# Kernel optimization log

Hardware: AMD Instinct MI355X
Metric: run time of the kernel (lower is better)

Reference implementation:

```python
import jax, jax.numpy as jnp
import numpy as np


def setup_inputs() -> dict:
    key = jax.random.key(0)
    ks = jax.random.split(key, 9)
    b, t_q, t_k, n_q, n_k = 4, 128, 512, 512, 512
    out_size = 512
    s = 0.02  # small init scale for weights
    return {
        "query": jax.random.normal(ks[0], (b, t_q, n_q), jnp.float32),
        "keys": jax.random.normal(ks[1], (b, t_k, n_k), jnp.float32),
        "values": jax.random.normal(ks[2], (b, t_k, n_k), jnp.float32),
        "W_q": jax.random.normal(ks[3], (n_k, n_q), jnp.float32) * s,
        "b_q": jnp.zeros((n_k,), jnp.float32),
        "w_att": jax.random.normal(ks[4], (n_k,), jnp.float32) * s,
        "b_att": jnp.zeros((1,), jnp.float32),
        "W_out": jax.random.normal(ks[5], (out_size, n_q + n_k), jnp.float32) * s,
        "b_out": jnp.zeros((out_size,), jnp.float32),
    }


def reference(query, keys, values, W_q, b_q, w_att, b_att, W_out, b_out):
    # linear_q: [b, t_q, query_size] -> [b, t_q, key_size]
    att_query = jnp.einsum("bqd,nd->bqn", query, W_q) + b_q
    # Bahdanau additive score: tanh(q + k) projected by linear_att (key_size -> 1)
    # intermediate: [b, t_q, t_k, n]
    sum_qk = jnp.tanh(att_query[:, :, None, :] + keys[:, None, :, :])
    scores = jnp.einsum("bqkn,n->bqk", sum_qk, w_att) + b_att[0]
    # mask is None by default; dropout p=0 -> identity
    probs = jax.nn.softmax(scores, axis=-1)  # [b, t_q, t_k]
    context = jnp.einsum("bqk,bkn->bqn", probs, values)
    # linear_out on concat([query, context]) + tanh nonlinearity
    cat = jnp.concatenate([query, context], axis=-1)
    out = jnp.tanh(jnp.einsum("bqc,oc->bqo", cat, W_out) + b_out)
    return out, probs
```

## Files before the change

### kernel.cpp

```cpp
#include <hip/hip_runtime.h>
#include <hip/hip_fp16.h>


#define BB    4
#define TQ    128
#define TK    512
#define NN    512
#define OUTSZ 512
#define CATSZ 1024
#define K2E   2.8853900817779268f
#define L2E   1.4426950408889634f
#define MAT   262144
#define WS_HALVES (11 * MAT)

typedef __attribute__((ext_vector_type(4))) _Float16 half4;
typedef __attribute__((ext_vector_type(8))) _Float16 half8;
typedef __attribute__((ext_vector_type(2))) _Float16 h2;

#if __has_builtin(__builtin_amdgcn_exp2f)
#define EXP2F(x) __builtin_amdgcn_exp2f(x)
#else
#define EXP2F(x) exp2f(x)
#endif
#if __has_builtin(__builtin_amdgcn_rcpf)
#define RCPF(x) __builtin_amdgcn_rcpf(x)
#else
#define RCPF(x) (1.0f / (x))
#endif

__device__ __forceinline__ h2 u2h(unsigned int u) {
  union { unsigned int i; h2 h; } v; v.i = u; return v.h;
}
__device__ __forceinline__ half4 uu2h4(unsigned int a, unsigned int b) {
  union { uint2 u; half4 h; } c; c.u = make_uint2(a, b); return c.h;
}
#if __has_builtin(__builtin_amdgcn_fdot2)
__device__ __forceinline__ float FDOT2(h2 a, h2 b, float c) {
  return __builtin_amdgcn_fdot2(a, b, c, false);
}
#else
__device__ __forceinline__ float FDOT2(h2 a, h2 b, float c) {
  return fmaf((float)a.x, (float)b.x, fmaf((float)a.y, (float)b.y, c));
}
#endif

__device__ __forceinline__ float fast_tanh(float x) {
  float e = EXP2F(x * K2E);
  return fmaf(-2.0f, RCPF(e + 1.0f), 1.0f);
}
__device__ __forceinline__ float waveRedSum(float s) {
  #pragma unroll
  for (int m = 32; m >= 1; m >>= 1) s += __shfl_xor(s, m, 64);
  return s;
}
__device__ __forceinline__ float fma4(float4 w, float4 v, float acc) {
  acc = fmaf(w.x, v.x, acc); acc = fmaf(w.y, v.y, acc);
  acc = fmaf(w.z, v.z, acc); acc = fmaf(w.w, v.w, acc);
  return acc;
}
__device__ __forceinline__ float4 scqh(float4 s, half4 E, float A, float w) {
  s.x = fmaf(w, RCPF(fmaf((float)E.x, A, 1.0f)), s.x);
  s.y = fmaf(w, RCPF(fmaf((float)E.y, A, 1.0f)), s.y);
  s.z = fmaf(w, RCPF(fmaf((float)E.z, A, 1.0f)), s.z);
  s.w = fmaf(w, RCPF(fmaf((float)E.w, A, 1.0f)), s.w);
  return s;
}
__device__ __forceinline__ void dotq(float4& r0, float4& r1, uint4 wp, unsigned int cpa, unsigned int cpb) {
  h2 c0 = u2h(cpa), c1 = u2h(cpb);
  r0.x = FDOT2(u2h(wp.x), c0, r0.x); r1.x = FDOT2(u2h(wp.x), c1, r1.x);
  r0.y = FDOT2(u2h(wp.y), c0, r0.y); r1.y = FDOT2(u2h(wp.y), c1, r1.y);
  r0.z = FDOT2(u2h(wp.z), c0, r0.z); r1.z = FDOT2(u2h(wp.z), c1, r1.z);
  r0.w = FDOT2(u2h(wp.w), c0, r0.w); r1.w = FDOT2(u2h(wp.w), c1, r1.w);
}

__global__ __launch_bounds__(256)
void pack_kernel(const float* __restrict__ keys, const float* __restrict__ W_q,
                 const float* __restrict__ W_out, const float* __restrict__ values,
                 _Float16* __restrict__ ws)
{
  __shared__ float tile[32][33];
  const int idx = blockIdx.x;
  const int tx = threadIdx.x & 31, ty = threadIdx.x >> 5;

  if (idx >= 1792) {
    int r = idx - 1792;
    int b = r >> 8, k2 = r & 255;
    const float* r0 = values + ((size_t)b * 512 + 2 * k2) * 512;
    const float* r1 = r0 + 512;
    int n0 = threadIdx.x * 2;
    float2 a = *(const float2*)(r0 + n0);
    float2 c = *(const float2*)(r1 + n0);
    _Float16* dst = ws + (size_t)7 * MAT + (size_t)b * MAT + k2 * 1024 + n0 * 2;
    half4 h = {(_Float16)a.x, (_Float16)c.x, (_Float16)a.y, (_Float16)c.y};
    *(half4*)dst = h;
    return;
  }

  if (idx < 1024) {
    int b = idx >> 8, r = idx & 255;
    int by = r >> 4, bx = r & 15;
    const float* src = keys + (size_t)b * MAT;
    _Float16* dst = ws + (size_t)b * MAT;
    #pragma unroll
    for (int i = 0; i < 32; i += 8)
      tile[ty + i][tx] = src[(size_t)(by * 32 + ty + i) * 512 + bx * 32 + tx] * K2E;
    __syncthreads();
    #pragma unroll
    for (int i = 0; i < 32; i += 8)
      dst[(size_t)(bx * 32 + ty + i) * 512 + by * 32 + tx] = (_Float16)EXP2F(tile[tx][ty + i]);
    return;
  }

  const float* src; _Float16* dst; int N; int by, bx;
  if (idx < 1280) {
    int r = idx - 1024; by = r >> 4; bx = r & 15;
    src = W_q; dst = ws + (size_t)4 * MAT; N = 512;
  } else {
    int r = idx - 1280; by = r >> 5; bx = r & 31;
    src = W_out; dst = ws + (size_t)5 * MAT; N = 1024;
  }
  #pragma unroll
  for (int i = 0; i < 32; i += 8)
    tile[ty + i][tx] = src[(size_t)(by * 32 + ty + i) * N + bx * 32 + tx];
  __syncthreads();
  #pragma unroll
  for (int i = 0; i < 32; i += 8) {
    int d = bx * 32 + ty + i;
    int o = by * 32 + tx;
    dst[(size_t)(d >> 1) * 1024 + o * 2 + (d & 1)] = (_Float16)tile[tx][ty + i];
  }
}

__global__ __launch_bounds__(1024, 4)
void attn_main(const float* __restrict__ query,
               const float* __restrict__ b_q, const float* __restrict__ w_att,
               const float* __restrict__ b_att, const float* __restrict__ b_out,
               const _Float16* __restrict__ ws,
               float* __restrict__ out, float* __restrict__ probs)
{
  __shared__ __align__(16) _Float16 catH[2048];
  __shared__ __align__(16) _Float16 pawF[NN * 4];
  __shared__ __align__(16) _Float16 prH[1024];
  __shared__ __align__(16) float  pt[8][2][NN];
  __shared__ float reds2[2][8];

  _Float16* ptH = (_Float16*)pt;

  const _Float16* wsKeys  = ws;
  const _Float16* wsWqP   = ws + (size_t)4 * MAT;
  const _Float16* wsWoutP = ws + (size_t)5 * MAT;
  const _Float16* wsValP  = ws + (size_t)7 * MAT;

  const int t    = threadIdx.x;
  const int qh   = t >> 9;
  const int u    = t & 511;
  const int G    = t >> 7;
  const int v    = t & 127;
  const int G16  = t >> 6;
  const int v6   = t & 63;
  const int wave = t >> 6, lane = t & 63, wq8 = wave & 7;

  const int p  = blockIdx.x;
  const int b  = (p & 7) >> 1;
  const int qg = ((p >> 3) << 1) | (p & 1);
  const int qabs0 = qg * 2;

  if (qh == 0) {
    float q0 = query[((size_t)(b * TQ + qabs0 + 0)) * NN + u];
    float q1 = query[((size_t)(b * TQ + qabs0 + 1)) * NN + u];
    catH[(u >> 1) * 4 + (u & 1)]     = (_Float16)q0;
    catH[(u >> 1) * 4 + 2 + (u & 1)] = (_Float16)q1;
  }
  __syncthreads();

  {
    const _Float16* wq = wsWqP + 8 * v;
    float4 a0 = {0,0,0,0}, a1 = {0,0,0,0};
    #pragma unroll 2
    for (int j2 = 0; j2 < 32; j2 += 2) {
      int d2 = 32 * G + j2;
      uint4 wp0 = *(const uint4*)(wq + (size_t)d2 * 1024);
      uint4 wp1 = *(const uint4*)(wq + (size_t)(d2 + 1) * 1024);
      uint4 cp2 = *(const uint4*)(&catH[d2 * 4]);
      dotq(a0, a1, wp0, cp2.x, cp2.y);
      dotq(a0, a1, wp1, cp2.z, cp2.w);
    }
    *(float4*)(&pt[G][0][4 * v]) = a0;
    *(float4*)(&pt[G][1][4 * v]) = a1;
  }
  __syncthreads();
  {
    float s = pt[0][qh][u] + pt[1][qh][u] + pt[2][qh][u] + pt[3][qh][u]
            + pt[4][qh][u] + pt[5][qh][u] + pt[6][qh][u] + pt[7][qh][u];
    float A = EXP2F(K2E * (s + b_q[u]));
    if (qh == 0) {
      pawF[u * 4 + 0] = (_Float16)A;
      pawF[u * 4 + 2] = (_Float16)w_att[u];
      pawF[u * 4 + 3] = (_Float16)0.f;
    } else {
      pawF[u * 4 + 1] = (_Float16)A;
    }
  }
  __syncthreads();

  {
    const _Float16* ke = wsKeys + (size_t)b * MAT + 8 * v6;
    float4 s0a = {0,0,0,0}, s0b = {0,0,0,0};
    float4 s1a = {0,0,0,0}, s1b = {0,0,0,0};
    #pragma unroll 2
    for (int j = 0; j < 32; j += 2) {
      int n = 32 * G16 + j;
      uint4 Eu0 = *(const uint4*)(ke + (size_t)n * 512);
      uint4 Eu1 = *(const uint4*)(ke + (size_t)(n + 1) * 512);
      uint4 pw  = *(const uint4*)(&pawF[n * 4]);
      h2 Aab = u2h(pw.x);  float w0f = (float)u2h(pw.y).x;
      h2 Acd = u2h(pw.z);  float w1f = (float)u2h(pw.w).x;
      float A0n = (float)Aab.x, A1n = (float)Aab.y;
      float A0m = (float)Acd.x, A1m = (float)Acd.y;
      half4 E0lo = uu2h4(Eu0.x, Eu0.y), E0hi = uu2h4(Eu0.z, Eu0.w);
      half4 E1lo = uu2h4(Eu1.x, Eu1.y), E1hi = uu2h4(Eu1.z, Eu1.w);
      s0a = scqh(s0a, E0lo, A0n, w0f);
      s0b = scqh(s0b, E0hi, A0n, w0f);
      s1a = scqh(s1a, E0lo, A1n, w0f);
      s1b = scqh(s1b, E0hi, A1n, w0f);
      s0a = scqh(s0a, E1lo, A0m, w1f);
      s0b = scqh(s0b, E1hi, A0m, w1f);
      s1a = scqh(s1a, E1lo, A1m, w1f);
      s1b = scqh(s1b, E1hi, A1m, w1f);
    }
    half8 w0 = {(_Float16)s0a.x, (_Float16)s0a.y, (_Float16)s0a.z, (_Float16)s0a.w,
                (_Float16)s0b.x, (_Float16)s0b.y, (_Float16)s0b.z, (_Float16)s0b.w};
    half8 w1 = {(_Float16)s1a.x, (_Float16)s1a.y, (_Float16)s1a.z, (_Float16)s1a.w,
                (_Float16)s1b.x, (_Float16)s1b.y, (_Float16)s1b.z, (_Float16)s1b.w};
    *(half8*)(ptH + (size_t)G16 * 512 + 8 * v6)        = w0;
    *(half8*)(ptH + 8192 + (size_t)G16 * 512 + 8 * v6) = w1;
  }
  __syncthreads();

  {
    const _Float16* pp = ptH + qh * 8192 + u;
    float s = 0.f;
    #pragma unroll
    for (int g = 0; g < 16; ++g)
      s += (float)pp[g * 512];
    float e = EXP2F(-K2E * s);
    float se = waveRedSum(e);
    if (lane == 0) reds2[qh][wq8] = se;
    __syncthreads();
    float bs = reds2[qh][0]+reds2[qh][1]+reds2[qh][2]+reds2[qh][3]
             + reds2[qh][4]+reds2[qh][5]+reds2[qh][6]+reds2[qh][7];
    float pv = e * RCPF(bs);
    prH[(u >> 1) * 4 + qh * 2 + (u & 1)] = (_Float16)pv;
    probs[((size_t)(b * TQ + qabs0 + qh)) * TK + u] = pv;
  }
  __syncthreads();

  {
    const _Float16* vp = wsValP + (size_t)b * MAT + 8 * v;
    float4 c0 = {0,0,0,0}, c1 = {0,0,0,0};
    #pragma unroll 2
    for (int j2 = 0; j2 < 32; j2 += 2) {
      int k2 = 32 * G + j2;
      uint4 vk0 = *(const uint4*)(vp + (size_t)k2 * 1024);
      uint4 vk1 = *(const uint4*)(vp + (size_t)(k2 + 1) * 1024);
      uint4 pp2 = *(const uint4*)(&prH[k2 * 4]);
      dotq(c0, c1, vk0, pp2.x, pp2.y);
      dotq(c0, c1, vk1, pp2.z, pp2.w);
    }
    *(float4*)(&pt[G][0][4 * v]) = c0;
    *(float4*)(&pt[G][1][4 * v]) = c1;
  }
  __syncthreads();
  {
    float s = pt[0][qh][u] + pt[1][qh][u] + pt[2][qh][u] + pt[3][qh][u]
            + pt[4][qh][u] + pt[5][qh][u] + pt[6][qh][u] + pt[7][qh][u];
    catH[(256 + (u >> 1)) * 4 + qh * 2 + (u & 1)] = (_Float16)s;
  }
  __syncthreads();

  {
    const _Float16* wo = wsWoutP + 8 * v;
    float4 o0 = {0,0,0,0}, o1 = {0,0,0,0};
    #pragma unroll 2
    for (int j2 = 0; j2 < 64; j2 += 2) {
      int c2 = 64 * G + j2;
      uint4 wp0 = *(const uint4*)(wo + (size_t)c2 * 1024);
      uint4 wp1 = *(const uint4*)(wo + (size_t)(c2 + 1) * 1024);
      uint4 cp2 = *(const uint4*)(&catH[c2 * 4]);
      dotq(o0, o1, wp0, cp2.x, cp2.y);
      dotq(o0, o1, wp1, cp2.z, cp2.w);
    }
    *(float4*)(&pt[G][0][4 * v]) = o0;
    *(float4*)(&pt[G][1][4 * v]) = o1;
  }
  __syncthreads();
  {
    float s = pt[0][qh][u] + pt[1][qh][u] + pt[2][qh][u] + pt[3][qh][u]
            + pt[4][qh][u] + pt[5][qh][u] + pt[6][qh][u] + pt[7][qh][u];
    float oo = s + b_out[u];
    out[((size_t)(b * TQ + qabs0 + qh)) * OUTSZ + u] = fast_tanh(oo);
  }
}

__device__ __forceinline__ float sc4f(float4 w, float4 k, float4 a, float acc) {
  acc = fmaf(w.x, RCPF(EXP2F(fmaf(k.x, K2E, a.x)) + 1.0f), acc);
  acc = fmaf(w.y, RCPF(EXP2F(fmaf(k.y, K2E, a.y)) + 1.0f), acc);
  acc = fmaf(w.z, RCPF(EXP2F(fmaf(k.z, K2E, a.z)) + 1.0f), acc);
  acc = fmaf(w.w, RCPF(EXP2F(fmaf(k.w, K2E, a.w)) + 1.0f), acc);
  return acc;
}

__global__ __launch_bounds__(1024, 4)
void attn_fallback(const float* __restrict__ query, const float* __restrict__ keys,
                   const float* __restrict__ values, const float* __restrict__ W_q,
                   const float* __restrict__ b_q, const float* __restrict__ w_att,
                   const float* __restrict__ b_att, const float* __restrict__ W_out,
                   const float* __restrict__ b_out,
                   float* __restrict__ out, float* __restrict__ probs)
{
  __shared__ __align__(16) float qv[2][NN];
  __shared__ __align__(16) float aqc[2][NN];
  __shared__ __align__(16) float wv[NN];
  __shared__ __align__(16) float pr[2][TK];
  __shared__ __align__(16) float ctx[2][NN];
  __shared__ __align__(16) float part[2][2][NN];
  __shared__ float redm[2][8], reds[2][8], redw[8];

  const int t = threadIdx.x, H = t >> 9, u = t & 511;
  const int wave = t >> 6, lane = t & 63, wq8 = wave & 7;
  const int p = blockIdx.x, b = (p & 7) >> 1;
  const int qg = ((p >> 3) << 1) | (p & 1), qabs0 = qg * 2;
  const float batt = b_att[0];

  if (H == 0) wv[u] = w_att[u];
  qv[H][u] = query[((size_t)(b * TQ + qabs0 + H)) * NN + u];
  __syncthreads();
  if (H == 0) {
    float wp = waveRedSum(wv[u]);
    if (lane == 0) redw[wq8] = wp;
  }
  __syncthreads();
  const float sumW = redw[0]+redw[1]+redw[2]+redw[3]+redw[4]+redw[5]+redw[6]+redw[7];

  {
    const float4* wq4 = (const float4*)(W_q + (size_t)u * NN + 256 * H);
    const float4* x4  = (const float4*)(qv[0] + 256 * H);
    const float4* y4  = (const float4*)(qv[1] + 256 * H);
    float a0=0.f, a0b=0.f, a1=0.f, a1b=0.f;
    #pragma unroll 2
    for (int c = 0; c < 16; ++c) {
      float4 wA=wq4[4*c+0], wB=wq4[4*c+1], wC=wq4[4*c+2], wD=wq4[4*c+3];
      float4 xA=x4[4*c+0], xB=x4[4*c+1], xC=x4[4*c+2], xD=x4[4*c+3];
      a0 = fma4(wA,xA,a0); a0b = fma4(wB,xB,a0b);
      a0 = fma4(wC,xC,a0); a0b = fma4(wD,xD,a0b);
      float4 yA=y4[4*c+0], yB=y4[4*c+1], yC=y4[4*c+2], yD=y4[4*c+3];
      a1 = fma4(wA,yA,a1); a1b = fma4(wB,yB,a1b);
      a1 = fma4(wC,yC,a1); a1b = fma4(wD,yD,a1b);
    }
    part[H][0][u] = a0 + a0b; part[H][1][u] = a1 + a1b;
  }
  __syncthreads();
  aqc[H][u] = (part[0][H][u] + part[1][H][u] + b_q[u]) * K2E;
  __syncthreads();

  {
    const float4* kr  = (const float4*)(keys + ((size_t)(b * TK) + u) * NN + 256 * H);
    const float4* a0p = (const float4*)(aqc[0] + 256 * H);
    const float4* a1p = (const float4*)(aqc[1] + 256 * H);
    const float4* w4  = (const float4*)(wv + 256 * H);
    float s0 = 0.f, s1 = 0.f;
    #pragma unroll 2
    for (int c = 0; c < 16; ++c) {
      float4 kA=kr[4*c+0], kB=kr[4*c+1], kC=kr[4*c+2], kD=kr[4*c+3];
      float4 wA=w4[4*c+0], wB=w4[4*c+1], wC=w4[4*c+2], wD=w4[4*c+3];
      float4 aA=a0p[4*c+0], aB=a0p[4*c+1], aC=a0p[4*c+2], aD=a0p[4*c+3];
      s0 = sc4f(wA,kA,aA,s0); s0 = sc4f(wB,kB,aB,s0);
      s0 = sc4f(wC,kC,aC,s0); s0 = sc4f(wD,kD,aD,s0);
      float4 bA=a1p[4*c+0], bB=a1p[4*c+1], bC=a1p[4*c+2], bD=a1p[4*c+3];
      s1 = sc4f(wA,kA,bA,s1); s1 = sc4f(wB,kB,bB,s1);
      s1 = sc4f(wC,kC,bC,s1); s1 = sc4f(wD,kD,bD,s1);
    }
    part[H][0][u] = s0; part[H][1][u] = s1;
  }
  __syncthreads();

  {
    float sc = batt + sumW - 2.0f * (part[0][H][u] + part[1][H][u]);
    float m = sc;
    #pragma unroll
    for (int mm = 32; mm >= 1; mm >>= 1) m = fmaxf(m, __shfl_xor(m, mm, 64));
    if (lane == 0) redm[H][wq8] = m;
    __syncthreads();
    float bm = fmaxf(fmaxf(fmaxf(redm[H][0],redm[H][1]),fmaxf(redm[H][2],redm[H][3])),
                     fmaxf(fmaxf(redm[H][4],redm[H][5]),fmaxf(redm[H][6],redm[H][7])));
    float e = EXP2F((sc - bm) * L2E);
    float se = waveRedSum(e);
    if (lane == 0) reds[H][wq8] = se;
    __syncthreads();
    float bs = reds[H][0]+reds[H][1]+reds[H][2]+reds[H][3]
             + reds[H][4]+reds[H][5]+reds[H][6]+reds[H][7];
    float pv = e * RCPF(bs);
    pr[H][u] = pv;
    probs[((size_t)(b * TQ + qabs0 + H)) * TK + u] = pv;
  }
  __syncthreads();

  {
    const float* vcol = values + ((size_t)(b * TK) + 256 * H) * NN + u;
    const float4* p0 = (const float4*)(pr[0] + 256 * H);
    const float4* p1 = (const float4*)(pr[1] + 256 * H);
    float c0a=0.f, c0b=0.f, c1a=0.f, c1b=0.f;
    #pragma unroll 2
    for (int k = 0; k < 256; k += 8) {
      float v0 = vcol[(size_t)(k+0)*NN]; float v1 = vcol[(size_t)(k+1)*NN];
      float v2 = vcol[(size_t)(k+2)*NN]; float v3 = vcol[(size_t)(k+3)*NN];
      float v4 = vcol[(size_t)(k+4)*NN]; float v5 = vcol[(size_t)(k+5)*NN];
      float v6 = vcol[(size_t)(k+6)*NN]; float v7 = vcol[(size_t)(k+7)*NN];
      float4 pA = p0[k>>2], pB = p0[(k>>2)+1];
      float4 qA = p1[k>>2], qB = p1[(k>>2)+1];
      c0a = fmaf(pA.x,v0,c0a); c0a = fmaf(pA.y,v1,c0a);
      c0b = fmaf(pA.z,v2,c0b); c0b = fmaf(pA.w,v3,c0b);
      c0a = fmaf(pB.x,v4,c0a); c0a = fmaf(pB.y,v5,c0a);
      c0b = fmaf(pB.z,v6,c0b); c0b = fmaf(pB.w,v7,c0b);
      c1a = fmaf(qA.x,v0,c1a); c1a = fmaf(qA.y,v1,c1a);
      c1b = fmaf(qA.z,v2,c1b); c1b = fmaf(qA.w,v3,c1b);
      c1a = fmaf(qB.x,v4,c1a); c1a = fmaf(qB.y,v5,c1a);
      c1b = fmaf(qB.z,v6,c1b); c1b = fmaf(qB.w,v7,c1b);
    }
    part[H][0][u] = c0a + c0b; part[H][1][u] = c1a + c1b;
  }
  __syncthreads();
  ctx[H][u] = part[0][H][u] + part[1][H][u];
  __syncthreads();

  {
    const float4* wo = (const float4*)(W_out + (size_t)u * CATSZ + 512 * H);
    const float4* x4 = (H == 0) ? (const float4*)qv[0] : (const float4*)ctx[0];
    const float4* y4 = (H == 0) ? (const float4*)qv[1] : (const float4*)ctx[1];
    float o0=0.f, o0b=0.f, o1=0.f, o1b=0.f;
    #pragma unroll 2
    for (int c = 0; c < 32; ++c) {
      float4 wA=wo[4*c+0], wB=wo[4*c+1], wC=wo[4*c+2], wD=wo[4*c+3];
      float4 xA=x4[4*c+0], xB=x4[4*c+1], xC=x4[4*c+2], xD=x4[4*c+3];
      o0 = fma4(wA,xA,o0); o0b = fma4(wB,xB,o0b);
      o0 = fma4(wC,xC,o0); o0b = fma4(wD,xD,o0b);
      float4 yA=y4[4*c+0], yB=y4[4*c+1], yC=y4[4*c+2], yD=y4[4*c+3];
      o1 = fma4(wA,yA,o1); o1b = fma4(wB,yB,o1b);
      o1 = fma4(wC,yC,o1); o1b = fma4(wD,yD,o1b);
    }
    part[H][0][u] = o0 + o0b; part[H][1][u] = o1 + o1b;
  }
  __syncthreads();
  {
    float oo = part[0][H][u] + part[1][H][u] + b_out[u];
    out[((size_t)(b * TQ + qabs0 + H)) * OUTSZ + u] = fast_tanh(oo);
  }
}

extern "C" void kernel_launch(void* const* d_in, const int* in_sizes, int n_in,
                              void* d_out, int out_size, void* d_ws, size_t ws_size,
                              hipStream_t stream) {
  const float* query = (const float*)d_in[0];
  const float* keys  = (const float*)d_in[1];
  const float* vals  = (const float*)d_in[2];
  const float* W_q   = (const float*)d_in[3];
  const float* b_q   = (const float*)d_in[4];
  const float* w_att = (const float*)d_in[5];
  const float* b_att = (const float*)d_in[6];
  const float* W_out = (const float*)d_in[7];
  const float* b_out = (const float*)d_in[8];

  float* out   = (float*)d_out;
  float* probs = out + (size_t)BB * TQ * OUTSZ;

  if (ws_size >= (size_t)WS_HALVES * sizeof(_Float16)) {
    _Float16* ws = (_Float16*)d_ws;
    pack_kernel<<<dim3(2816), dim3(256), 0, stream>>>(keys, W_q, W_out, vals, ws);
    attn_main<<<dim3(BB * TQ / 2), dim3(1024), 0, stream>>>(
        query, b_q, w_att, b_att, b_out, ws, out, probs);
  } else {
    attn_fallback<<<dim3(BB * TQ / 2), dim3(1024), 0, stream>>>(
        query, keys, vals, W_q, b_q, w_att, b_att, W_out, b_out, out, probs);
  }
}
```

Measured before the change: 115.8 us.

## Split query and output projections into separate kernels that batch four query pairs

The monolithic attention kernel is split into three kernels: a query-projection kernel, a middle scoring/softmax/context kernel, and an output-projection kernel. The two projection kernels each handle four query pairs per block and split the output dimension across four blocks, so every W_q/W_out element loaded is reused across eight query rows instead of two. Intermediates (packed query/context, A/w_att pairs) now pass through the global workspace, which is enlarged. This trades two extra launches and extra global round-trips for less weight traffic per block.

```diff
diff --git a/kernel.cpp b/kernel.cpp
--- a/kernel.cpp
+++ b/kernel.cpp
@@ -11,7 +11,7 @@
 #define K2E   2.8853900817779268f
 #define L2E   1.4426950408889634f
 #define MAT   262144
-#define WS_HALVES (11 * MAT)
+#define WS_HALVES (15 * MAT)
 
 typedef __attribute__((ext_vector_type(4))) _Float16 half4;
 typedef __attribute__((ext_vector_type(8))) _Float16 half8;
@@ -74,13 +74,28 @@
 }
 
 __global__ __launch_bounds__(256)
-void pack_kernel(const float* __restrict__ keys, const float* __restrict__ W_q,
+void pack_kernel(const float* __restrict__ query,
+                 const float* __restrict__ keys, const float* __restrict__ W_q,
                  const float* __restrict__ W_out, const float* __restrict__ values,
                  _Float16* __restrict__ ws)
 {
   __shared__ float tile[32][33];
   const int idx = blockIdx.x;
   const int tx = threadIdx.x & 31, ty = threadIdx.x >> 5;
+
+  if (idx >= 2816) {
+    int p = idx - 2816;
+    int b = (p & 7) >> 1;
+    int qg = ((p >> 3) << 1) | (p & 1);
+    const float* q0 = query + ((size_t)(b * TQ + qg * 2)) * NN;
+    const float* q1 = q0 + NN;
+    int cp = threadIdx.x;
+    float2 a = *(const float2*)(q0 + 2 * cp);
+    float2 c = *(const float2*)(q1 + 2 * cp);
+    half4 h = {(_Float16)a.x, (_Float16)a.y, (_Float16)c.x, (_Float16)c.y};
+    *(half4*)(ws + (size_t)11 * MAT + (size_t)p * 2048 + 4 * cp) = h;
+    return;
+  }
 
   if (idx >= 1792) {
     int r = idx - 1792;
@@ -132,13 +147,63 @@
 }
 
 __global__ __launch_bounds__(1024, 4)
-void attn_main(const float* __restrict__ query,
-               const float* __restrict__ b_q, const float* __restrict__ w_att,
-               const float* __restrict__ b_att, const float* __restrict__ b_out,
-               const _Float16* __restrict__ ws,
-               float* __restrict__ out, float* __restrict__ probs)
+void attq_kernel(const float* __restrict__ b_q, const float* __restrict__ w_att,
+                 _Float16* __restrict__ ws)
 {
-  __shared__ __align__(16) _Float16 catH[2048];
+  __shared__ __align__(16) _Float16 ldsQ[4][1024];
+  __shared__ __align__(16) float pt[8][4][2][128];
+
+  const _Float16* wsWqP = ws + (size_t)4 * MAT;
+  const _Float16* catG  = ws + (size_t)11 * MAT;
+  _Float16* pawG        = ws + (size_t)13 * MAT;
+
+  const int t = threadIdx.x, bx = blockIdx.x;
+  const int ng = bx & 3, pg = bx >> 2;
+
+  if (t < 512) {
+    int qp = t >> 7, j = t & 127;
+    ((uint4*)&ldsQ[qp][0])[j] =
+        ((const uint4*)(catG + (size_t)(4 * pg + qp) * 2048))[j];
+  }
+  __syncthreads();
+
+  const int G = t >> 7, pq = (t >> 5) & 3, v5 = t & 31;
+  {
+    const _Float16* wq = wsWqP + 8 * (32 * ng + v5);
+    float4 a0 = {0,0,0,0}, a1 = {0,0,0,0};
+    #pragma unroll 2
+    for (int j2 = 0; j2 < 32; j2 += 2) {
+      int d2 = 32 * G + j2;
+      uint4 wp0 = *(const uint4*)(wq + (size_t)d2 * 1024);
+      uint4 wp1 = *(const uint4*)(wq + (size_t)(d2 + 1) * 1024);
+      uint4 cp2 = *(const uint4*)(&ldsQ[pq][d2 * 4]);
+      dotq(a0, a1, wp0, cp2.x, cp2.y);
+      dotq(a0, a1, wp1, cp2.z, cp2.w);
+    }
+    *(float4*)(&pt[G][pq][0][4 * v5]) = a0;
+    *(float4*)(&pt[G][pq][1][4 * v5]) = a1;
+  }
+  __syncthreads();
+  {
+    int pq2 = t >> 8, row = (t >> 7) & 1, no = t & 127;
+    int n = 128 * ng + no;
+    float s = pt[0][pq2][row][no] + pt[1][pq2][row][no]
+            + pt[2][pq2][row][no] + pt[3][pq2][row][no]
+            + pt[4][pq2][row][no] + pt[5][pq2][row][no]
+            + pt[6][pq2][row][no] + pt[7][pq2][row][no];
+    float A = EXP2F(K2E * (s + b_q[n]));
+    _Float16* dst = pawG + (size_t)(4 * pg + pq2) * 2048 + 4 * n;
+    dst[row] = (_Float16)A;
+    if (row == 0) {
+      dst[2] = (_Float16)w_att[n];
+      dst[3] = (_Float16)0.f;
+    }
+  }
+}
+
+__global__ __launch_bounds__(1024, 4)
+void attn_mid(_Float16* __restrict__ ws, float* __restrict__ probs)
+{
   __shared__ __align__(16) _Float16 pawF[NN * 4];
   __shared__ __align__(16) _Float16 prH[1024];
   __shared__ __align__(16) float  pt[8][2][NN];
@@ -146,10 +211,10 @@
 
   _Float16* ptH = (_Float16*)pt;
 
-  const _Float16* wsKeys  = ws;
-  const _Float16* wsWqP   = ws + (size_t)4 * MAT;
-  const _Float16* wsWoutP = ws + (size_t)5 * MAT;
-  const _Float16* wsValP  = ws + (size_t)7 * MAT;
+  const _Float16* wsKeys = ws;
+  const _Float16* wsValP = ws + (size_t)7 * MAT;
+  _Float16* catG         = ws + (size_t)11 * MAT;
+  const _Float16* pawG   = ws + (size_t)13 * MAT;
 
   const int t    = threadIdx.x;
   const int qh   = t >> 9;
@@ -165,42 +230,7 @@
   const int qg = ((p >> 3) << 1) | (p & 1);
   const int qabs0 = qg * 2;
 
-  if (qh == 0) {
-    float q0 = query[((size_t)(b * TQ + qabs0 + 0)) * NN + u];
-    float q1 = query[((size_t)(b * TQ + qabs0 + 1)) * NN + u];
-    catH[(u >> 1) * 4 + (u & 1)]     = (_Float16)q0;
-    catH[(u >> 1) * 4 + 2 + (u & 1)] = (_Float16)q1;
-  }
-  __syncthreads();
-
-  {
-    const _Float16* wq = wsWqP + 8 * v;
-    float4 a0 = {0,0,0,0}, a1 = {0,0,0,0};
-    #pragma unroll 2
-    for (int j2 = 0; j2 < 32; j2 += 2) {
-      int d2 = 32 * G + j2;
-      uint4 wp0 = *(const uint4*)(wq + (size_t)d2 * 1024);
-      uint4 wp1 = *(const uint4*)(wq + (size_t)(d2 + 1) * 1024);
-      uint4 cp2 = *(const uint4*)(&catH[d2 * 4]);
-      dotq(a0, a1, wp0, cp2.x, cp2.y);
-      dotq(a0, a1, wp1, cp2.z, cp2.w);
-    }
-    *(float4*)(&pt[G][0][4 * v]) = a0;
-    *(float4*)(&pt[G][1][4 * v]) = a1;
-  }
-  __syncthreads();
-  {
-    float s = pt[0][qh][u] + pt[1][qh][u] + pt[2][qh][u] + pt[3][qh][u]
-            + pt[4][qh][u] + pt[5][qh][u] + pt[6][qh][u] + pt[7][qh][u];
-    float A = EXP2F(K2E * (s + b_q[u]));
-    if (qh == 0) {
-      pawF[u * 4 + 0] = (_Float16)A;
-      pawF[u * 4 + 2] = (_Float16)w_att[u];
-      pawF[u * 4 + 3] = (_Float16)0.f;
-    } else {
-      pawF[u * 4 + 1] = (_Float16)A;
-    }
-  }
+  ((unsigned int*)pawF)[t] = ((const unsigned int*)(pawG + (size_t)p * 2048))[t];
   __syncthreads();
 
   {
@@ -274,31 +304,55 @@
   {
     float s = pt[0][qh][u] + pt[1][qh][u] + pt[2][qh][u] + pt[3][qh][u]
             + pt[4][qh][u] + pt[5][qh][u] + pt[6][qh][u] + pt[7][qh][u];
-    catH[(256 + (u >> 1)) * 4 + qh * 2 + (u & 1)] = (_Float16)s;
-  }
-  __syncthreads();
-
-  {
-    const _Float16* wo = wsWoutP + 8 * v;
+    catG[(size_t)p * 2048 + (size_t)(256 + (u >> 1)) * 4 + qh * 2 + (u & 1)] =
+        (_Float16)s;
+  }
+}
+
+__global__ __launch_bounds__(1024, 4)
+void out_kernel(const float* __restrict__ b_out, const _Float16* __restrict__ ws,
+                float* __restrict__ out)
+{
+  __shared__ __align__(16) _Float16 ldsCat[8192];
+  __shared__ __align__(16) float pt[8][4][2][128];
+
+  const _Float16* wsWoutP = ws + (size_t)5 * MAT;
+  const _Float16* catG    = ws + (size_t)11 * MAT;
+
+  const int t = threadIdx.x, bx = blockIdx.x;
+  const int og = bx & 3, pg = bx >> 2;
+
+  ((uint4*)ldsCat)[t] = ((const uint4*)(catG + (size_t)4 * pg * 2048))[t];
+  __syncthreads();
+
+  const int G = t >> 7, pq = (t >> 5) & 3, v5 = t & 31;
+  {
+    const _Float16* wo = wsWoutP + 8 * (32 * og + v5);
     float4 o0 = {0,0,0,0}, o1 = {0,0,0,0};
     #pragma unroll 2
     for (int j2 = 0; j2 < 64; j2 += 2) {
       int c2 = 64 * G + j2;
       uint4 wp0 = *(const uint4*)(wo + (size_t)c2 * 1024);
       uint4 wp1 = *(const uint4*)(wo + (size_t)(c2 + 1) * 1024);
-      uint4 cp2 = *(const uint4*)(&catH[c2 * 4]);
+      uint4 cp2 = *(const uint4*)(&ldsCat[pq * 2048 + c2 * 4]);
       dotq(o0, o1, wp0, cp2.x, cp2.y);
       dotq(o0, o1, wp1, cp2.z, cp2.w);
     }
-    *(float4*)(&pt[G][0][4 * v]) = o0;
-    *(float4*)(&pt[G][1][4 * v]) = o1;
-  }
-  __syncthreads();
-  {
-    float s = pt[0][qh][u] + pt[1][qh][u] + pt[2][qh][u] + pt[3][qh][u]
-            + pt[4][qh][u] + pt[5][qh][u] + pt[6][qh][u] + pt[7][qh][u];
-    float oo = s + b_out[u];
-    out[((size_t)(b * TQ + qabs0 + qh)) * OUTSZ + u] = fast_tanh(oo);
+    *(float4*)(&pt[G][pq][0][4 * v5]) = o0;
+    *(float4*)(&pt[G][pq][1][4 * v5]) = o1;
+  }
+  __syncthreads();
+  {
+    int pq2 = t >> 8, row = (t >> 7) & 1, oo = t & 127;
+    float s = pt[0][pq2][row][oo] + pt[1][pq2][row][oo]
+            + pt[2][pq2][row][oo] + pt[3][pq2][row][oo]
+            + pt[4][pq2][row][oo] + pt[5][pq2][row][oo]
+            + pt[6][pq2][row][oo] + pt[7][pq2][row][oo];
+    int o = 128 * og + oo;
+    int p = 4 * pg + pq2;
+    int b = (p & 7) >> 1;
+    int qg = ((p >> 3) << 1) | (p & 1);
+    out[((size_t)(b * TQ + qg * 2 + row)) * OUTSZ + o] = fast_tanh(s + b_out[o]);
   }
 }
 
@@ -475,9 +529,10 @@
 
   if (ws_size >= (size_t)WS_HALVES * sizeof(_Float16)) {
     _Float16* ws = (_Float16*)d_ws;
-    pack_kernel<<<dim3(2816), dim3(256), 0, stream>>>(keys, W_q, W_out, vals, ws);
-    attn_main<<<dim3(BB * TQ / 2), dim3(1024), 0, stream>>>(
-        query, b_q, w_att, b_att, b_out, ws, out, probs);
+    pack_kernel<<<dim3(3072), dim3(256), 0, stream>>>(query, keys, W_q, W_out, vals, ws);
+    attq_kernel<<<dim3(256), dim3(1024), 0, stream>>>(b_q, w_att, ws);
+    attn_mid<<<dim3(BB * TQ / 2), dim3(1024), 0, stream>>>(ws, probs);
+    out_kernel<<<dim3(256), dim3(1024), 0, stream>>>(b_out, ws, out);
   } else {
     attn_fallback<<<dim3(BB * TQ / 2), dim3(1024), 0, stream>>>(
         query, keys, vals, W_q, b_q, w_att, b_att, W_out, b_out, out, probs);
```

Result: no change. 118.1 us (+1.9%).
